# Optimization experiments

Hardware: AMD Instinct MI355X
Metric: run time of the kernel (lower is better)

Reference implementation:

```python
import jax, jax.numpy as jnp
import numpy as np

EPS = 1e-12  # torch F.normalize eps

def setup_inputs() -> dict:
    key = jax.random.key(0)
    k1, k2, k3, k4 = jax.random.split(key, 4)
    B, S, T, D, r = 8, 50, 77, 1024, 16
    h = jax.random.normal(k1, (B, S, T, D), dtype=jnp.float32)
    # R init: randn / sqrt(D), matching the torch module
    R = jax.random.normal(k2, (S, r, D), dtype=jnp.float32) / np.sqrt(D).astype(np.float32)
    # W, b are zero-init in the module; use small random values so the edit is non-trivial
    W = jax.random.normal(k3, (S, r, D), dtype=jnp.float32) * 0.02
    b = jax.random.normal(k4, (S, r), dtype=jnp.float32) * 0.02
    return {"h": h, "R": R, "W": W, "b": b}

def reference(h, R, W, b):
    # h: (B, S, T, D); R, W: (S, r, D); b: (S, r)
    # Per step t: Phi(h_t) = h_t + Rn_t^T (W_t h_t + b_t - Rn_t h_t), Rn = row-normalized R
    norm = jnp.sqrt(jnp.sum(R * R, axis=-1, keepdims=True))
    Rn = R / jnp.maximum(norm, EPS)
    Rh = jnp.einsum('bstd,srd->bstr', h, Rn)
    Wh = jnp.einsum('bstd,srd->bstr', h, W) + b[None, :, None, :]
    delta = jnp.einsum('bstr,srd->bstd', Wh - Rh, Rn)
    return h + delta
```

## Files before the change

### kernel.cpp

```cpp
#include <hip/hip_runtime.h>


typedef __attribute__((ext_vector_type(8))) short short8;
typedef __attribute__((ext_vector_type(4))) float floatx4;

__device__ __forceinline__ short f2bf(float f) {
  unsigned u = __float_as_uint(f);
  u += 0x7fffu + ((u >> 16) & 1u);
  return (short)(u >> 16);
}

#define S_ 50
#define T_ 77
#define NTOK 616

__global__ __launch_bounds__(256, 2) void loreft_main(
    const float* __restrict__ hG, const float* __restrict__ RG,
    const float* __restrict__ WG, const float* __restrict__ bG,
    float* __restrict__ outG) {
  __shared__ short Ml[16 * 1024];
  __shared__ short Rt[1024 * 16];

  const int s = blockIdx.x;
  const int tid = threadIdx.x;
  const int lane = tid & 63;
  const int wvi = tid >> 6;
  const int m16 = lane & 15;
  const int quad = lane >> 4;

#pragma unroll
  for (int rr = 0; rr < 4; ++rr) {
    const int r = wvi * 4 + rr;
    const floatx4* Rrow = (const floatx4*)(RG + (size_t)((s * 16 + r) << 10));
    const floatx4* Wrow = (const floatx4*)(WG + (size_t)((s * 16 + r) << 10));
    floatx4 rv0 = Rrow[lane * 4 + 0];
    floatx4 rv1 = Rrow[lane * 4 + 1];
    floatx4 rv2 = Rrow[lane * 4 + 2];
    floatx4 rv3 = Rrow[lane * 4 + 3];
    float ss = 0.f;
#pragma unroll
    for (int j = 0; j < 4; ++j)
      ss += rv0[j] * rv0[j] + rv1[j] * rv1[j] + rv2[j] * rv2[j] + rv3[j] * rv3[j];
#pragma unroll
    for (int m = 1; m < 64; m <<= 1) ss += __shfl_xor(ss, m);
    const float inv = 1.0f / fmaxf(sqrtf(ss), 1e-12f);

    floatx4 wa0 = Wrow[lane * 4 + 0];
    floatx4 wa1 = Wrow[lane * 4 + 1];
    floatx4 wa2 = Wrow[lane * 4 + 2];
    floatx4 wa3 = Wrow[lane * 4 + 3];
    float rn[16];
    short8 m0, m1;
#pragma unroll
    for (int j = 0; j < 4; ++j) {
      rn[j]      = rv0[j] * inv;  m0[j]     = f2bf(wa0[j] - rn[j]);
      rn[4 + j]  = rv1[j] * inv;  m0[4 + j] = f2bf(wa1[j] - rn[4 + j]);
      rn[8 + j]  = rv2[j] * inv;  m1[j]     = f2bf(wa2[j] - rn[8 + j]);
      rn[12 + j] = rv3[j] * inv;  m1[4 + j] = f2bf(wa3[j] - rn[12 + j]);
    }
    *(short8*)(Ml + r * 1024 + (((2 * lane) ^ (r & 7)) << 3)) = m0;
    *(short8*)(Ml + r * 1024 + (((2 * lane + 1) ^ (r & 7)) << 3)) = m1;
#pragma unroll
    for (int jj = 0; jj < 16; ++jj)
      Rt[((lane * 16 + jj) << 4) + r] = f2bf(rn[jj]);
  }
  __syncthreads();

  const int tokbase = blockIdx.y * 64 + wvi * 16;
  int tokA = tokbase + m16; if (tokA > NTOK - 1) tokA = NTOK - 1;
  const int bb1 = tokA / T_;
  const int tt1 = tokA - bb1 * T_;
  const size_t rowoff = ((size_t)((bb1 * S_ + s) * T_ + tt1)) << 10;
  const float* hrow = hG + rowoff;
  const floatx4* hrow4 = (const floatx4*)hrow;
  const short* mrow = Ml + m16 * 1024;
  const int msw = m16 & 7;

  floatx4 acc = {0.f, 0.f, 0.f, 0.f};
#pragma unroll 4
  for (int kb = 0; kb < 32; ++kb) {
    floatx4 p0 = hrow4[kb * 8 + quad * 2];
    floatx4 p1 = hrow4[kb * 8 + quad * 2 + 1];
    short8 af;
#pragma unroll
    for (int j = 0; j < 4; ++j) { af[j] = f2bf(p0[j]); af[4 + j] = f2bf(p1[j]); }
    short8 bf = *(const short8*)(mrow + (((kb * 4 + quad) ^ msw) << 3));
    acc = __builtin_amdgcn_mfma_f32_16x16x32_bf16(af, bf, acc, 0, 0, 0);
  }

  const float bias = bG[s * 16 + m16];
  float cf[4];
#pragma unroll
  for (int i = 0; i < 4; ++i) cf[i] = acc[i] + bias;

  unsigned lo = ((unsigned)(unsigned short)f2bf(cf[0])) |
                (((unsigned)(unsigned short)f2bf(cf[1])) << 16);
  unsigned hi = ((unsigned)(unsigned short)f2bf(cf[2])) |
                (((unsigned)(unsigned short)f2bf(cf[3])) << 16);
  short8 bfrag;
  {
    const int srcbase = ((m16 >> 2) << 4) + ((quad & 1) << 3);
    const int regsel = m16 & 3;
#pragma unroll
    for (int j = 0; j < 8; ++j) {
      unsigned vlo = __shfl(lo, srcbase + j);
      unsigned vhi = __shfl(hi, srcbase + j);
      unsigned v32 = (regsel & 2) ? vhi : vlo;
      bfrag[j] = (short)((regsel & 1) ? (v32 >> 16) : (v32 & 0xffffu));
    }
  }
  const short8 zero8 = {0, 0, 0, 0, 0, 0, 0, 0};
  if (quad >= 2) bfrag = zero8;

  float* orow = outG + rowoff;
  const bool valE = (tokbase + m16) < NTOK;
  const int q16 = (quad & 1) << 3;

#pragma unroll 4
  for (int dt = 0; dt < 64; ++dt) {
    short8 t = *(const short8*)(Rt + ((dt * 16 + m16) << 4) + q16);
    short8 ar = (quad < 2) ? t : zero8;
    floatx4 z = {0.f, 0.f, 0.f, 0.f};
    floatx4 dv = __builtin_amdgcn_mfma_f32_16x16x32_bf16(ar, bfrag, z, 0, 0, 0);
    const int d0 = dt * 16 + quad * 4;
    if (valE) {
      floatx4 hv = *(const floatx4*)(hrow + d0);
      floatx4 o;
#pragma unroll
      for (int i = 0; i < 4; ++i) o[i] = hv[i] + dv[i];
      *(floatx4*)(orow + d0) = o;
    }
  }
}

extern "C" void kernel_launch(void* const* d_in, const int* in_sizes, int n_in,
                              void* d_out, int out_size, void* d_ws, size_t ws_size,
                              hipStream_t stream) {
  const float* h = (const float*)d_in[0];
  const float* R = (const float*)d_in[1];
  const float* W = (const float*)d_in[2];
  const float* b = (const float*)d_in[3];
  dim3 grid(S_, 10);
  loreft_main<<<grid, 256, 0, stream>>>(h, R, W, b, (float*)d_out);
}
```

Measured before the change: 257.9 us.

## Split weight prep into separate kernel and read bf16 weights from global

Moves the R normalization, W-Rn difference and transposed Rn packing into a separate prep kernel that writes bf16 weight buffers to workspace once per step slot. The main kernel then drops its 64KB of shared memory and per-block redundant prep, which was repeated across 10 token blocks, and loads weight fragments directly from global/L2. It also uses nontemporal loads and stores for the streaming h reread and output write, and adds an early exit for empty waves. The cost is an extra kernel launch and global reads of weights in place of LDS reads.

```diff
diff --git a/kernel.cpp b/kernel.cpp
--- a/kernel.cpp
+++ b/kernel.cpp
@@ -14,19 +14,14 @@
 #define T_ 77
 #define NTOK 616
 
-__global__ __launch_bounds__(256, 2) void loreft_main(
-    const float* __restrict__ hG, const float* __restrict__ RG,
-    const float* __restrict__ WG, const float* __restrict__ bG,
-    float* __restrict__ outG) {
-  __shared__ short Ml[16 * 1024];
-  __shared__ short Rt[1024 * 16];
-
+__global__ __launch_bounds__(256) void loreft_prep(
+    const float* __restrict__ RG, const float* __restrict__ WG,
+    short* __restrict__ Mg, short* __restrict__ Rg) {
+  __shared__ float RnL[16][1024];
   const int s = blockIdx.x;
   const int tid = threadIdx.x;
   const int lane = tid & 63;
   const int wvi = tid >> 6;
-  const int m16 = lane & 15;
-  const int quad = lane >> 4;
 
 #pragma unroll
   for (int rr = 0; rr < 4; ++rr) {
@@ -58,23 +53,49 @@
       rn[8 + j]  = rv2[j] * inv;  m1[j]     = f2bf(wa2[j] - rn[8 + j]);
       rn[12 + j] = rv3[j] * inv;  m1[4 + j] = f2bf(wa3[j] - rn[12 + j]);
     }
-    *(short8*)(Ml + r * 1024 + (((2 * lane) ^ (r & 7)) << 3)) = m0;
-    *(short8*)(Ml + r * 1024 + (((2 * lane + 1) ^ (r & 7)) << 3)) = m1;
+    short* mdst = Mg + (size_t)(s * 16 + r) * 1024 + lane * 16;
+    *(short8*)mdst = m0;
+    *(short8*)(mdst + 8) = m1;
 #pragma unroll
-    for (int jj = 0; jj < 16; ++jj)
-      Rt[((lane * 16 + jj) << 4) + r] = f2bf(rn[jj]);
+    for (int jj = 0; jj < 16; ++jj) RnL[r][lane * 16 + jj] = rn[jj];
   }
   __syncthreads();
 
+#pragma unroll
+  for (int dd = 0; dd < 4; ++dd) {
+    const int d = dd * 256 + tid;
+    short8 lo8, hi8;
+#pragma unroll
+    for (int rj = 0; rj < 8; ++rj) {
+      lo8[rj] = f2bf(RnL[rj][d]);
+      hi8[rj] = f2bf(RnL[rj + 8][d]);
+    }
+    short* dst = Rg + ((size_t)s * 1024 + d) * 16;
+    *(short8*)dst = lo8;
+    *(short8*)(dst + 8) = hi8;
+  }
+}
+
+__global__ __launch_bounds__(256, 2) void loreft_main(
+    const float* __restrict__ hG, const float* __restrict__ bG,
+    const short* __restrict__ Mg, const short* __restrict__ Rg,
+    float* __restrict__ outG) {
+  const int tid = threadIdx.x;
+  const int lane = tid & 63;
+  const int wvi = tid >> 6;
+  const int m16 = lane & 15;
+  const int quad = lane >> 4;
+  const int s = blockIdx.x;
+
   const int tokbase = blockIdx.y * 64 + wvi * 16;
+  if (tokbase >= NTOK) return;
   int tokA = tokbase + m16; if (tokA > NTOK - 1) tokA = NTOK - 1;
   const int bb1 = tokA / T_;
   const int tt1 = tokA - bb1 * T_;
   const size_t rowoff = ((size_t)((bb1 * S_ + s) * T_ + tt1)) << 10;
   const float* hrow = hG + rowoff;
   const floatx4* hrow4 = (const floatx4*)hrow;
-  const short* mrow = Ml + m16 * 1024;
-  const int msw = m16 & 7;
+  const short* mrow = Mg + (size_t)(s * 16 + m16) * 1024 + quad * 8;
 
   floatx4 acc = {0.f, 0.f, 0.f, 0.f};
 #pragma unroll 4
@@ -84,7 +105,7 @@
     short8 af;
 #pragma unroll
     for (int j = 0; j < 4; ++j) { af[j] = f2bf(p0[j]); af[4 + j] = f2bf(p1[j]); }
-    short8 bf = *(const short8*)(mrow + (((kb * 4 + quad) ^ msw) << 3));
+    short8 bf = *(const short8*)(mrow + kb * 32);
     acc = __builtin_amdgcn_mfma_f32_16x16x32_bf16(af, bf, acc, 0, 0, 0);
   }
 
@@ -115,20 +136,21 @@
   float* orow = outG + rowoff;
   const bool valE = (tokbase + m16) < NTOK;
   const int q16 = (quad & 1) << 3;
+  const short* rbase = Rg + (size_t)s * (1024 * 16) + q16;
 
-#pragma unroll 4
+#pragma unroll 8
   for (int dt = 0; dt < 64; ++dt) {
-    short8 t = *(const short8*)(Rt + ((dt * 16 + m16) << 4) + q16);
-    short8 ar = (quad < 2) ? t : zero8;
+    short8 ar = zero8;
+    if (quad < 2) ar = *(const short8*)(rbase + (dt * 16 + m16) * 16);
     floatx4 z = {0.f, 0.f, 0.f, 0.f};
     floatx4 dv = __builtin_amdgcn_mfma_f32_16x16x32_bf16(ar, bfrag, z, 0, 0, 0);
     const int d0 = dt * 16 + quad * 4;
     if (valE) {
-      floatx4 hv = *(const floatx4*)(hrow + d0);
+      floatx4 hv = __builtin_nontemporal_load((const floatx4*)(hrow + d0));
       floatx4 o;
 #pragma unroll
       for (int i = 0; i < 4; ++i) o[i] = hv[i] + dv[i];
-      *(floatx4*)(orow + d0) = o;
+      __builtin_nontemporal_store(o, (floatx4*)(orow + d0));
     }
   }
 }
@@ -140,6 +162,8 @@
   const float* R = (const float*)d_in[1];
   const float* W = (const float*)d_in[2];
   const float* b = (const float*)d_in[3];
-  dim3 grid(S_, 10);
-  loreft_main<<<grid, 256, 0, stream>>>(h, R, W, b, (float*)d_out);
+  short* Mg = (short*)d_ws;
+  short* Rg = Mg + (size_t)S_ * 16 * 1024;
+  loreft_prep<<<dim3(S_), 256, 0, stream>>>(R, W, Mg, Rg);
+  loreft_main<<<dim3(S_, 10), 256, 0, stream>>>(h, b, Mg, Rg, (float*)d_out);
 }
```

Measured after the change: 328.3 us. 1.27x slower.
